# Kernel optimization log

Hardware: AMD Instinct MI355X
Metric: run time of the kernel (lower is better)

## Reference

```python
import jax, jax.numpy as jnp
import numpy as np

K, D = 32, 256

def setup_inputs() -> dict:
    key = jax.random.key(0)
    k1, k2 = jax.random.split(key)
    batch_weights = jax.random.normal(k1, (2048, K), dtype=jnp.float32)
    archs = jax.random.normal(k2, (K, D, D), dtype=jnp.float32)
    return {"batch_weights": batch_weights, "archs": archs}

def reference(batch_weights, archs):
    d = archs.shape[-1]
    # off-diagonal mask: ones(d) - eye(d)
    mask = jnp.ones((d, d), dtype=archs.dtype) - jnp.eye(d, dtype=archs.dtype)
    archetypes = archs * mask  # (k, d, d), diagonal zeroed
    # out[b] = sum_k w[b,k] * archetypes[k]  -> single batched contraction
    return jnp.einsum('bk,kde->bde', batch_weights, archetypes)
```

## Files before the change

### kernel.cpp

```cpp
#include <hip/hip_runtime.h>
#include <hip/hip_bf16.h>


typedef float vfloat4 __attribute__((ext_vector_type(4)));

constexpr int K = 32;
constexpr int D = 256;
constexpr int N = D * D;
constexpr int NPT = 4;
constexpr int THREADS = 256;
constexpr int N_CHUNK = THREADS * NPT;
constexpr int B_CHUNK = 128;

__global__ __launch_bounds__(THREADS, 1)
void explainer_kernel(const float* __restrict__ w,
                      const float* __restrict__ archs,
                      float* __restrict__ out,
                      int B) {
    const int nbase = blockIdx.x * N_CHUNK + threadIdx.x * NPT;
    const int bbase = blockIdx.y * B_CHUNK;

    float a[K][NPT];
#pragma unroll
    for (int k = 0; k < K; ++k) {
        const vfloat4 v = *reinterpret_cast<const vfloat4*>(archs + (size_t)k * N + nbase);
        a[k][0] = v.x; a[k][1] = v.y; a[k][2] = v.z; a[k][3] = v.w;
    }
#pragma unroll
    for (int j = 0; j < NPT; ++j) {
        if (((nbase + j) % 257) == 0) {
#pragma unroll
            for (int k = 0; k < K; ++k) a[k][j] = 0.0f;
        }
    }

    const int bend = min(bbase + B_CHUNK, B);
    for (int b = bbase; b < bend; ++b) {
        const float* __restrict__ wb = w + (size_t)b * K;
        float acc0 = 0.f, acc1 = 0.f, acc2 = 0.f, acc3 = 0.f;
#pragma unroll
        for (int k = 0; k < K; ++k) {
            const float wk = wb[k];
            acc0 = fmaf(wk, a[k][0], acc0);
            acc1 = fmaf(wk, a[k][1], acc1);
            acc2 = fmaf(wk, a[k][2], acc2);
            acc3 = fmaf(wk, a[k][3], acc3);
        }
        vfloat4 o; o.x = acc0; o.y = acc1; o.z = acc2; o.w = acc3;
        __builtin_nontemporal_store(o, reinterpret_cast<vfloat4*>(out + (size_t)b * N + nbase));
    }
}

extern "C" void kernel_launch(void* const* d_in, const int* in_sizes, int n_in,
                              void* d_out, int out_size, void* d_ws, size_t ws_size,
                              hipStream_t stream) {
    const float* w     = (const float*)d_in[0];
    const float* archs = (const float*)d_in[1];
    float* out = (float*)d_out;

    const int B = in_sizes[0] / K;
    const int grid_x = N / N_CHUNK;
    const int grid_y = (B + B_CHUNK - 1) / B_CHUNK;

    dim3 grid(grid_x, grid_y);
    dim3 block(THREADS);
    explainer_kernel<<<grid, block, 0, stream>>>(w, archs, out, B);
}
```

Before: 614.5 us.

## Prefetch weight rows as float4 vectors and raise occupancy hint

Loads each batch row of weights as float4 vectors and prefetches the next row while computing the current one. It raises the launch-bounds hint to allow more resident blocks per CU, and replaces nontemporal output stores with regular stores. The intent is to hide weight-load latency and improve overlap of output writes. The risks are register pressure from the double-buffered weights under the tighter launch bound, and cache pollution from the normal stores.

```diff
diff --git a/kernel.cpp b/kernel.cpp
--- a/kernel.cpp
+++ b/kernel.cpp
@@ -1,5 +1,4 @@
 #include <hip/hip_runtime.h>
-#include <hip/hip_bf16.h>
 
 
 typedef float vfloat4 __attribute__((ext_vector_type(4)));
@@ -12,7 +11,7 @@
 constexpr int N_CHUNK = THREADS * NPT;
 constexpr int B_CHUNK = 128;
 
-__global__ __launch_bounds__(THREADS, 1)
+__global__ __launch_bounds__(THREADS, 3)
 void explainer_kernel(const float* __restrict__ w,
                       const float* __restrict__ archs,
                       float* __restrict__ out,
@@ -35,19 +34,50 @@
     }
 
     const int bend = min(bbase + B_CHUNK, B);
+
+    const vfloat4* __restrict__ wv = reinterpret_cast<const vfloat4*>(w);
+
+    vfloat4 wcur[K / 4];
+#pragma unroll
+    for (int q = 0; q < K / 4; ++q) wcur[q] = wv[(size_t)bbase * (K / 4) + q];
+
+    float* __restrict__ optr = out + (size_t)bbase * N + nbase;
+
     for (int b = bbase; b < bend; ++b) {
-        const float* __restrict__ wb = w + (size_t)b * K;
+        const int bn = (b + 1 < bend) ? (b + 1) : b;
+        vfloat4 wnext[K / 4];
+#pragma unroll
+        for (int q = 0; q < K / 4; ++q) wnext[q] = wv[(size_t)bn * (K / 4) + q];
+
         float acc0 = 0.f, acc1 = 0.f, acc2 = 0.f, acc3 = 0.f;
 #pragma unroll
-        for (int k = 0; k < K; ++k) {
-            const float wk = wb[k];
-            acc0 = fmaf(wk, a[k][0], acc0);
-            acc1 = fmaf(wk, a[k][1], acc1);
-            acc2 = fmaf(wk, a[k][2], acc2);
-            acc3 = fmaf(wk, a[k][3], acc3);
+        for (int q = 0; q < K / 4; ++q) {
+            const vfloat4 wq = wcur[q];
+            acc0 = fmaf(wq.x, a[4 * q + 0][0], acc0);
+            acc1 = fmaf(wq.x, a[4 * q + 0][1], acc1);
+            acc2 = fmaf(wq.x, a[4 * q + 0][2], acc2);
+            acc3 = fmaf(wq.x, a[4 * q + 0][3], acc3);
+            acc0 = fmaf(wq.y, a[4 * q + 1][0], acc0);
+            acc1 = fmaf(wq.y, a[4 * q + 1][1], acc1);
+            acc2 = fmaf(wq.y, a[4 * q + 1][2], acc2);
+            acc3 = fmaf(wq.y, a[4 * q + 1][3], acc3);
+            acc0 = fmaf(wq.z, a[4 * q + 2][0], acc0);
+            acc1 = fmaf(wq.z, a[4 * q + 2][1], acc1);
+            acc2 = fmaf(wq.z, a[4 * q + 2][2], acc2);
+            acc3 = fmaf(wq.z, a[4 * q + 2][3], acc3);
+            acc0 = fmaf(wq.w, a[4 * q + 3][0], acc0);
+            acc1 = fmaf(wq.w, a[4 * q + 3][1], acc1);
+            acc2 = fmaf(wq.w, a[4 * q + 3][2], acc2);
+            acc3 = fmaf(wq.w, a[4 * q + 3][3], acc3);
         }
-        vfloat4 o; o.x = acc0; o.y = acc1; o.z = acc2; o.w = acc3;
-        __builtin_nontemporal_store(o, reinterpret_cast<vfloat4*>(out + (size_t)b * N + nbase));
+
+        vfloat4 o;
+        o.x = acc0; o.y = acc1; o.z = acc2; o.w = acc3;
+        *reinterpret_cast<vfloat4*>(optr) = o;
+        optr += N;
+
+#pragma unroll
+        for (int q = 0; q < K / 4; ++q) wcur[q] = wnext[q];
     }
 }
 
```

New measurement: 626.1 us. Within noise of the previous version (+1.9%).
